# Optimization experiments

Measured on AMD Instinct MI355X. Metric: run time of the kernel, lower is better.

Reference implementation:

```python
import jax, jax.numpy as jnp
import numpy as np

NUM_HEADS = 16
DIM = 1024
HARMONICS = 32
B, L = 2, 2048


def holo_linear(x, basis, phase, amp):
    # x: [B,L,in]; basis: [H,in] (L2-normalized rows); phase/amp: [out,H]
    # Original builds complex(res,0) * amp*exp(i*phase) and takes real of sum
    # over harmonics -> sum_h res_h * amp[o,h]*cos(phase[o,h]).
    resonance = jnp.einsum('bli,hi->blh', x, basis)        # [B,L,H]
    w = amp * jnp.cos(phase)                               # [out,H]
    return jnp.einsum('blh,oh->blo', resonance, w)         # [B,L,out]


def setup_inputs() -> dict:
    key = jax.random.key(0)
    ks = jax.random.split(key, 13)
    two_pi = 2.0 * np.pi

    def make_proj(k0, k1):
        basis = jax.random.normal(k0, (HARMONICS, DIM), dtype=jnp.float32)
        basis = basis / jnp.linalg.norm(basis, axis=1, keepdims=True)
        phase = jax.random.normal(k1, (DIM, HARMONICS), dtype=jnp.float32) * two_pi
        amp = jnp.ones((DIM, HARMONICS), dtype=jnp.float32) / HARMONICS
        return basis, phase, amp

    x = jax.random.normal(ks[0], (B, L, DIM), dtype=jnp.float32)
    bq, pq, aq = make_proj(ks[1], ks[2])
    bk, pk, ak = make_proj(ks[3], ks[4])
    bv, pv, av = make_proj(ks[5], ks[6])
    bo, po, ao = make_proj(ks[7], ks[8])
    return {
        'x': x,
        'basis_q': bq, 'phase_q': pq, 'amp_q': aq,
        'basis_k': bk, 'phase_k': pk, 'amp_k': ak,
        'basis_v': bv, 'phase_v': pv, 'amp_v': av,
        'basis_o': bo, 'phase_o': po, 'amp_o': ao,
    }


def reference(x, basis_q, phase_q, amp_q, basis_k, phase_k, amp_k,
              basis_v, phase_v, amp_v, basis_o, phase_o, amp_o):
    Bsz, Ls, C = x.shape
    head_dim = C // NUM_HEADS
    scale = head_dim ** (-0.5)

    def split_heads(t):  # [B,L,C] -> [B,H,L,hd]
        return t.reshape(Bsz, Ls, NUM_HEADS, head_dim).transpose(0, 2, 1, 3)

    q = split_heads(holo_linear(x, basis_q, phase_q, amp_q))
    k = split_heads(holo_linear(x, basis_k, phase_k, amp_k))
    v = split_heads(holo_linear(x, basis_v, phase_v, amp_v))

    attn = jnp.einsum('bhqd,bhkd->bhqk', q, k) * scale      # [B,H,L,L]
    attn = jax.nn.softmax(attn, axis=-1)
    out = jnp.einsum('bhqk,bhkd->bhqd', attn, v)            # [B,H,L,hd]
    out = out.transpose(0, 2, 1, 3).reshape(Bsz, Ls, C)
    return holo_linear(out, basis_o, phase_o, amp_o)
```

## Files before the change

### kernel.cpp

```cpp
#include <hip/hip_runtime.h>
#include <hip/hip_bf16.h>
#include <cstdint>
#include <cstddef>

#define NH   16
#define HD   64
#define CD   1024
#define HARM 32
#define BSZ  2
#define LSEQ 2048
#define NROW (BSZ*LSEQ)

typedef __attribute__((ext_vector_type(8))) short short8;
typedef __attribute__((ext_vector_type(16))) float float16v;

__device__ inline ushort bf16u(float f) {
    __hip_bfloat16 h = __float2bfloat16(f);
    return *(ushort*)&h;
}
__device__ inline float ubf(ushort u) {
    return __uint_as_float((unsigned)u << 16);
}
__device__ inline unsigned pk2(float a, float b) {
    return (unsigned)bf16u(a) | ((unsigned)bf16u(b) << 16);
}
__device__ inline int crow(int r, int half) { return (r & 3) + 8 * (r >> 2) + 4 * half; }

union S8U { short8 v; uint2 u[2]; };

__device__ inline short8 pk_frag(const unsigned* pk, int cc) {
    S8U o;
    o.u[0] = make_uint2(pk[4 * cc + 0], pk[4 * cc + 1]);
    o.u[1] = make_uint2(pk[4 * cc + 2], pk[4 * cc + 3]);
    return o.v;
}

__global__ void prep_kern(const float* __restrict__ bq, const float* __restrict__ bk,
                          const float* __restrict__ bv, const float* __restrict__ bo,
                          const float* __restrict__ pq, const float* __restrict__ aq,
                          const float* __restrict__ pk, const float* __restrict__ ak,
                          const float* __restrict__ pv, const float* __restrict__ av,
                          const float* __restrict__ po, const float* __restrict__ ao,
                          ushort* __restrict__ bF, ushort* __restrict__ wqkvF,
                          ushort* __restrict__ wobF) {
    const float QSCALE = 0.125f * 1.44269504088896340736f;
    unsigned tid = blockIdx.x * 256 + threadIdx.x;
    if (tid < 16384) {
        unsigned l31 = tid & 31, h = (tid >> 5) & 1, kc = (tid >> 6) & 63, proj = tid >> 12;
        const float* bp = (proj == 0) ? bq : (proj == 1) ? bk : (proj == 2) ? bv : bo;
        const float* s = bp + (size_t)l31 * CD + kc * 16;
        unsigned o0 = (proj == 3) ? h * 4 : h * 8;
        unsigned o1 = o0 + ((proj == 3) ? 8 : 4);
        float4 f0 = *(const float4*)(s + o0), f1 = *(const float4*)(s + o1);
        S8U o;
        o.u[0] = make_uint2(pk2(f0.x, f0.y), pk2(f0.z, f0.w));
        o.u[1] = make_uint2(pk2(f1.x, f1.y), pk2(f1.z, f1.w));
        *(short8*)(bF + (size_t)tid * 8) = o.v;
        return;
    }
    if (tid < 28672) {
        unsigned i = tid - 16384;
        unsigned l31 = i & 31, h = (i >> 5) & 1, kc2 = (i >> 6) & 1;
        unsigned ntp = (i >> 7) & 31, proj = i >> 12;
        const float* ph = (proj == 0) ? pq : (proj == 1) ? pk : pv;
        const float* am = (proj == 0) ? aq : (proj == 1) ? ak : av;
        float sc = (proj == 0) ? QSCALE : 1.0f;
        size_t s = (size_t)(ntp * 32 + l31) * HARM + kc2 * 16 + h * 4;
        float4 p0 = *(const float4*)(ph + s), p1 = *(const float4*)(ph + s + 8);
        float4 a0 = *(const float4*)(am + s), a1 = *(const float4*)(am + s + 8);
        S8U o;
        o.u[0] = make_uint2(pk2(a0.x * cosf(p0.x) * sc, a0.y * cosf(p0.y) * sc),
                            pk2(a0.z * cosf(p0.z) * sc, a0.w * cosf(p0.w) * sc));
        o.u[1] = make_uint2(pk2(a1.x * cosf(p1.x) * sc, a1.y * cosf(p1.y) * sc),
                            pk2(a1.z * cosf(p1.z) * sc, a1.w * cosf(p1.w) * sc));
        *(short8*)(wqkvF + (size_t)i * 8) = o.v;
        return;
    }
    {
        unsigned i = tid - 28672;
        unsigned l31 = i & 31, h = (i >> 5) & 1, kc2 = (i >> 6) & 1, nt = i >> 7;
        size_t s = (size_t)(nt * 32 + l31) * HARM + kc2 * 16 + h * 4;
        float4 p0 = *(const float4*)(po + s), p1 = *(const float4*)(po + s + 8);
        float4 a0 = *(const float4*)(ao + s), a1 = *(const float4*)(ao + s + 8);
        S8U o;
        o.u[0] = make_uint2(pk2(a0.x * cosf(p0.x), a0.y * cosf(p0.y)),
                            pk2(a0.z * cosf(p0.z), a0.w * cosf(p0.w)));
        o.u[1] = make_uint2(pk2(a1.x * cosf(p1.x), a1.y * cosf(p1.y)),
                            pk2(a1.z * cosf(p1.z), a1.w * cosf(p1.w)));
        *(short8*)(wobF + (size_t)i * 8) = o.v;
    }
}

__global__ __launch_bounds__(256) void res_part_kern(const float* __restrict__ x,
                                                     const ushort* __restrict__ bF,
                                                     float* __restrict__ respart) {
    __shared__ ushort xs[32 * 256];
    __shared__ float red[4 * 16 * 64];
    const int t = threadIdx.x, wave = t >> 6, lane = t & 63;
    const int l31 = lane & 31, h = lane >> 5;
    const int kseg = blockIdx.x & 3, rg = blockIdx.x >> 2;
    const int n0 = rg * 32;

#pragma unroll
    for (int i = 0; i < 8; i++) {
        int idx = i * 256 + t, row = idx >> 6, c4 = idx & 63;
        float4 v = *(const float4*)(x + (size_t)(n0 + row) * CD + kseg * 256 + c4 * 4);
        int chunk = (c4 >> 1) ^ (row & 15), sub = c4 & 1;
        *(ushort4*)(&xs[row * 256 + chunk * 8 + sub * 4]) =
            make_ushort4(bf16u(v.x), bf16u(v.y), bf16u(v.z), bf16u(v.w));
    }
    __syncthreads();

    float16v resC[3] = {};
#pragma unroll
    for (int kci = 0; kci < 4; kci++) {
        int c = wave * 8 + kci * 2 + h;
        short8 bx = *(const short8*)(&xs[l31 * 256 + (c ^ (l31 & 15)) * 8]);
        int kcg = kseg * 16 + wave * 4 + kci;
#pragma unroll
        for (int p = 0; p < 3; p++) {
            short8 a = *(const short8*)(bF + ((size_t)((p * 64 + kcg) * 2 + h) * 32 + l31) * 8);
            resC[p] = __builtin_amdgcn_mfma_f32_32x32x16_bf16(a, bx, resC[p], 0, 0, 0);
        }
    }
    float* outb = respart + ((size_t)(kseg * 128 + rg) * 3) * 1024;
    for (int p = 0; p < 3; p++) {
        __syncthreads();
#pragma unroll
        for (int r = 0; r < 16; r++) red[wave * 1024 + r * 64 + lane] = resC[p][r];
        __syncthreads();
#pragma unroll
        for (int i = 0; i < 4; i++) {
            int e = i * 256 + t;
            outb[p * 1024 + e] = (red[e] + red[1024 + e]) + (red[2048 + e] + red[3072 + e]);
        }
    }
}

__global__ __launch_bounds__(256) void rp_kern(const float* __restrict__ respart,
                                               unsigned* __restrict__ rfbuf) {
    const int tid = blockIdx.x * 256 + threadIdx.x;
    const int rest = tid / 384, u = tid % 384;
    const int p = u >> 7, cc = (u >> 6) & 1, lane = u & 63;

    const float* base = respart + ((size_t)rest * 3 + p) * 1024 + cc * 512 + lane;
    unsigned w[4];
#pragma unroll
    for (int q = 0; q < 4; q++) {
        const float* pa = base + (2 * q) * 64;
        const float* pb = pa + 64;
        float a = (pa[0] + pa[393216]) + (pa[2 * 393216] + pa[3 * 393216]);
        float bv_ = (pb[0] + pb[393216]) + (pb[2 * 393216] + pb[3 * 393216]);
        w[q] = pk2(a, bv_);
    }
    *(uint4*)(rfbuf + (size_t)rest * 1536 + ((p * 2 + cc) * 64 + lane) * 4) =
        make_uint4(w[0], w[1], w[2], w[3]);
}

__global__ __launch_bounds__(256) void qkv_kern(const unsigned* __restrict__ rfbuf,
                                                const ushort* __restrict__ wqkvF,
                                                ushort* __restrict__ qtile,
                                                ushort* __restrict__ ktile,
                                                ushort* __restrict__ vtile) {
    const int t = threadIdx.x, wave = t >> 6, lane = t & 63;
    const int l31 = lane & 31, h = lane >> 5;
    const int ntg = blockIdx.x % 24, rest = blockIdx.x / 24;
    const int b = rest >> 6, l0q = rest & 63;
    const int nt = ntg * 4 + wave;
    const int proj = nt >> 5, ntp = nt & 31;
    const int head = ntp >> 1, sub = ntp & 1;
    const int kblk = l0q >> 1, mtk = l0q & 1;

    const unsigned* rb = rfbuf + (size_t)rest * 1536 + ((proj * 2) * 64 + lane) * 4;
    uint4 q0 = *(const uint4*)(rb);
    uint4 q1 = *(const uint4*)(rb + 256);
    S8U r0, r1;
    r0.u[0] = make_uint2(q0.x, q0.y); r0.u[1] = make_uint2(q0.z, q0.w);
    r1.u[0] = make_uint2(q1.x, q1.y); r1.u[1] = make_uint2(q1.z, q1.w);

    const ushort* wp = wqkvF + ((size_t)(proj * 32 + ntp) * 4) * 256;
    short8 wf0 = *(const short8*)(wp + (size_t)h * 256 + l31 * 8);
    short8 wf1 = *(const short8*)(wp + (size_t)(2 + h) * 256 + l31 * 8);
    float16v c = {};
    if (proj < 2) {
        c = __builtin_amdgcn_mfma_f32_32x32x16_bf16(wf0, r0.v, c, 0, 0, 0);
        c = __builtin_amdgcn_mfma_f32_32x32x16_bf16(wf1, r1.v, c, 0, 0, 0);
    } else {
        c = __builtin_amdgcn_mfma_f32_32x32x16_bf16(r0.v, wf0, c, 0, 0, 0);
        c = __builtin_amdgcn_mfma_f32_32x32x16_bf16(r1.v, wf1, c, 0, 0, 0);
    }
    unsigned pkc[8];
#pragma unroll
    for (int j = 0; j < 8; j++) pkc[j] = pk2(c[2 * j], c[2 * j + 1]);

    if (proj == 0) {
        ushort* base = qtile + (((size_t)(b * NH + head) * 64 + l0q)) * 2048;
#pragma unroll
        for (int cc = 0; cc < 2; cc++)
            *(short8*)(base + (sub * 2 + cc) * 512 + h * 256 + l31 * 8) =
                pk_frag(pkc, cc);
    } else if (proj == 1) {
        ushort* base = ktile + ((size_t)(b * NH + head) * 32 + kblk) * 4096 + mtk * 2048;
#pragma unroll
        for (int cc = 0; cc < 2; cc++)
            *(short8*)(base + (sub * 2 + cc) * 512 + h * 256 + l31 * 8) =
                pk_frag(pkc, cc);
    } else {
        ushort* base = vtile + ((size_t)(b * NH + head) * 32 + kblk) * 4096 + sub * 2048;
#pragma unroll
        for (int cc = 0; cc < 2; cc++)
            *(short8*)(base + (mtk * 2 + cc) * 512 + h * 256 + l31 * 8) =
                pk_frag(pkc, cc);
    }
}

__global__ __launch_bounds__(256, 2) void flash8(const ushort* __restrict__ qtile,
                                                 const ushort* __restrict__ ktile,
                                                 const ushort* __restrict__ vtile,
                                                 ushort* __restrict__ Opart,
                                                 float* __restrict__ lbuf) {
    __shared__ ushort kb[2][4096];
    __shared__ ushort vb[2][4096];
    const int t = threadIdx.x;
    const int wave = t >> 6, lane = t & 63;
    const int l31 = lane & 31, h = lane >> 5;
    const int d = blockIdx.x;
    const int logical = (d & 7) * 64 + (d >> 3);
    const int bh = logical >> 4;
    const int inner = logical & 15;
    const int ksp = inner >> 3;
    const int qtg = inner & 7;
    const int qt0 = qtg * 8 + wave * 2;
    const int fo = h * 256 + l31 * 8;
    const int so = t * 8;

    const ushort* qtb = qtile + ((size_t)bh * 64 + qt0) * 2048;
    short8 qfa[4], qfb[4];
#pragma unroll
    for (int kc = 0; kc < 4; kc++) {
        qfa[kc] = *(const short8*)(qtb + kc * 512 + fo);
        qfb[kc] = *(const short8*)(qtb + 2048 + kc * 512 + fo);
    }

    const ushort* ktb = ktile + (size_t)bh * 32 * 4096;
    const ushort* vtb = vtile + (size_t)bh * 32 * 4096;
    const int k0 = ksp * 16;

    {
        const ushort* ks = ktb + (size_t)k0 * 4096;
        const ushort* vs = vtb + (size_t)k0 * 4096;
        short8 a0 = *(const short8*)(ks + so);
        short8 a1 = *(const short8*)(ks + 2048 + so);
        short8 b0 = *(const short8*)(vs + so);
        short8 b1 = *(const short8*)(vs + 2048 + so);
        *(short8*)(kb[0] + so) = a0; *(short8*)(kb[0] + 2048 + so) = a1;
        *(short8*)(vb[0] + so) = b0; *(short8*)(vb[0] + 2048 + so) = b1;
    }
    __syncthreads();

    S8U ones;
    ones.u[0] = make_uint2(0x3F803F80u, 0x3F803F80u);
    ones.u[1] = make_uint2(0x3F803F80u, 0x3F803F80u);

    float16v O0a = {}, O1a = {}, Laa = {};
    float16v O0b = {}, O1b = {}, Lab = {};

#pragma unroll
    for (int it = 0; it < 16; it++) {
        const int cur = it & 1, nxt = cur ^ 1;

        short8 a0, a1, b0, b1;
        if (it < 15) {
            const ushort* ks = ktb + (size_t)(k0 + it + 1) * 4096;
            const ushort* vs = vtb + (size_t)(k0 + it + 1) * 4096;
            a0 = *(const short8*)(ks + so);
            a1 = *(const short8*)(ks + 2048 + so);
            b0 = *(const short8*)(vs + so);
            b1 = *(const short8*)(vs + 2048 + so);
        }

        short8 kf[2][4];
#pragma unroll
        for (int mt = 0; mt < 2; mt++)
#pragma unroll
            for (int kc = 0; kc < 4; kc++)
                kf[mt][kc] = *(const short8*)(kb[cur] + mt * 2048 + kc * 512 + fo);
        float16v s0a = {}, s1a = {}, s0b = {}, s1b = {};
#pragma unroll
        for (int kc = 0; kc < 4; kc++) {
            s0a = __builtin_amdgcn_mfma_f32_32x32x16_bf16(kf[0][kc], qfa[kc], s0a, 0, 0, 0);
            s1a = __builtin_amdgcn_mfma_f32_32x32x16_bf16(kf[1][kc], qfa[kc], s1a, 0, 0, 0);
            s0b = __builtin_amdgcn_mfma_f32_32x32x16_bf16(kf[0][kc], qfb[kc], s0b, 0, 0, 0);
            s1b = __builtin_amdgcn_mfma_f32_32x32x16_bf16(kf[1][kc], qfb[kc], s1b, 0, 0, 0);
        }
        short8 vf[2][4];
#pragma unroll
        for (int mt = 0; mt < 2; mt++)
#pragma unroll
            for (int kc = 0; kc < 4; kc++)
                vf[mt][kc] = *(const short8*)(vb[cur] + mt * 2048 + kc * 512 + fo);

        unsigned pk0a[8], pk1a[8], pk0b[8], pk1b[8];
#pragma unroll
        for (int j2 = 0; j2 < 8; j2++) {
            pk0a[j2] = pk2(__builtin_amdgcn_exp2f(s0a[2 * j2]),
                           __builtin_amdgcn_exp2f(s0a[2 * j2 + 1]));
            pk1a[j2] = pk2(__builtin_amdgcn_exp2f(s1a[2 * j2]),
                           __builtin_amdgcn_exp2f(s1a[2 * j2 + 1]));
            pk0b[j2] = pk2(__builtin_amdgcn_exp2f(s0b[2 * j2]),
                           __builtin_amdgcn_exp2f(s0b[2 * j2 + 1]));
            pk1b[j2] = pk2(__builtin_amdgcn_exp2f(s1b[2 * j2]),
                           __builtin_amdgcn_exp2f(s1b[2 * j2 + 1]));
        }
#pragma unroll
        for (int kc = 0; kc < 4; kc++) {
            const unsigned* pma = (kc < 2) ? pk0a : pk1a;
            const unsigned* pmb = (kc < 2) ? pk0b : pk1b;
            short8 bfa = pk_frag(pma, kc & 1);
            short8 bfb = pk_frag(pmb, kc & 1);
            Laa = __builtin_amdgcn_mfma_f32_32x32x16_bf16(ones.v, bfa, Laa, 0, 0, 0);
            O0a = __builtin_amdgcn_mfma_f32_32x32x16_bf16(vf[0][kc], bfa, O0a, 0, 0, 0);
            O1a = __builtin_amdgcn_mfma_f32_32x32x16_bf16(vf[1][kc], bfa, O1a, 0, 0, 0);
            Lab = __builtin_amdgcn_mfma_f32_32x32x16_bf16(ones.v, bfb, Lab, 0, 0, 0);
            O0b = __builtin_amdgcn_mfma_f32_32x32x16_bf16(vf[0][kc], bfb, O0b, 0, 0, 0);
            O1b = __builtin_amdgcn_mfma_f32_32x32x16_bf16(vf[1][kc], bfb, O1b, 0, 0, 0);
        }

        if (it < 15) {
            *(short8*)(kb[nxt] + so) = a0; *(short8*)(kb[nxt] + 2048 + so) = a1;
            *(short8*)(vb[nxt] + so) = b0; *(short8*)(vb[nxt] + 2048 + so) = b1;
        }
        __syncthreads();
    }

    if (h == 0) {
        lbuf[(size_t)ksp * 65536 + bh * 2048 + qt0 * 32 + l31] = Laa[0];
        lbuf[(size_t)ksp * 65536 + bh * 2048 + (qt0 + 1) * 32 + l31] = Lab[0];
    }
#pragma unroll
    for (int j = 0; j < 2; j++) {
        ushort* ob = Opart + (size_t)ksp * 4194304 + ((size_t)bh * 64 + qt0 + j) * 2048;
#pragma unroll
        for (int mt = 0; mt < 2; mt++) {
            float16v Ov = j ? (mt ? O1b : O0b) : (mt ? O1a : O0a);
            unsigned pkO[8];
#pragma unroll
            for (int j2 = 0; j2 < 8; j2++) pkO[j2] = pk2(Ov[2 * j2], Ov[2 * j2 + 1]);
#pragma unroll
            for (int cc = 0; cc < 2; cc++)
                *(short8*)(ob + ((mt * 2 + cc) * 2 + h) * 256 + l31 * 8) =
                    pk_frag(pkO, cc);
        }
    }
}

__global__ __launch_bounds__(256) void back1_kern(const ushort* __restrict__ Opart,
                                                  const float* __restrict__ lbuf,
                                                  const ushort* __restrict__ bF,
                                                  float* __restrict__ respart2) {
    __shared__ float red[4 * 16 * 64];
    const int t = threadIdx.x, wave = t >> 6, lane = t & 63;
    const int l31 = lane & 31, h = lane >> 5;
    const int hq = blockIdx.x & 3, rg = blockIdx.x >> 2;
    const int b = rg >> 6, qt = rg & 63;
    const int hd = hq * 4 + wave, bh = b * NH + hd;

    float lb = lbuf[(size_t)bh * 2048 + qt * 32 + l31] +
               lbuf[(size_t)65536 + (size_t)bh * 2048 + qt * 32 + l31];
    float invl = 1.0f / lb;
    const ushort* ob0 = Opart + ((size_t)bh * 64 + qt) * 2048;
    const ushort* ob1 = ob0 + 4194304;

    float16v c = {};
#pragma unroll
    for (int kc = 0; kc < 4; kc++) {
        short8 o0 = *(const short8*)(ob0 + (kc * 2 + h) * 256 + l31 * 8);
        short8 o1 = *(const short8*)(ob1 + (kc * 2 + h) * 256 + l31 * 8);
        float av[8];
#pragma unroll
        for (int e = 0; e < 8; e++)
            av[e] = (ubf((ushort)o0[e]) + ubf((ushort)o1[e])) * invl;
        S8U bn;
        bn.u[0] = make_uint2(pk2(av[0], av[1]), pk2(av[2], av[3]));
        bn.u[1] = make_uint2(pk2(av[4], av[5]), pk2(av[6], av[7]));
        int kcg = hd * 4 + kc;
        short8 a = *(const short8*)(bF + ((size_t)((3 * 64 + kcg) * 2 + h) * 32 + l31) * 8);
        c = __builtin_amdgcn_mfma_f32_32x32x16_bf16(a, bn.v, c, 0, 0, 0);
    }
#pragma unroll
    for (int r = 0; r < 16; r++) red[wave * 1024 + r * 64 + lane] = c[r];
    __syncthreads();
#pragma unroll
    for (int i = 0; i < 4; i++) {
        int e = i * 256 + t;
        respart2[((size_t)hq * 128 + rg) * 1024 + e] =
            (red[e] + red[1024 + e]) + (red[2048 + e] + red[3072 + e]);
    }
}

__global__ __launch_bounds__(256) void back2_kern(const float* __restrict__ respart2,
                                                  const ushort* __restrict__ wobF,
                                                  float* __restrict__ out) {
    const int t = threadIdx.x, wave = t >> 6, lane = t & 63;
    const int l31 = lane & 31, h = lane >> 5;
    const int ng = blockIdx.x & 7, rg = blockIdx.x >> 3;

    float cf[16];
#pragma unroll
    for (int r = 0; r < 16; r++) {
        const float* pp = respart2 + r * 64 + lane;
        cf[r] = (pp[(size_t)rg * 1024] + pp[(size_t)(128 + rg) * 1024]) +
                (pp[(size_t)(256 + rg) * 1024] + pp[(size_t)(384 + rg) * 1024]);
    }
    unsigned pkr[8];
#pragma unroll
    for (int j = 0; j < 8; j++) pkr[j] = pk2(cf[2 * j], cf[2 * j + 1]);
    short8 a0 = pk_frag(pkr, 0);
    short8 a1 = pk_frag(pkr, 1);

    int nt = ng * 4 + wave;
    const ushort* wp = wobF + (size_t)nt * 1024;
    short8 wf0 = *(const short8*)(wp + (size_t)h * 256 + l31 * 8);
    short8 wf1 = *(const short8*)(wp + (size_t)(2 + h) * 256 + l31 * 8);
    float16v co = {};
    co = __builtin_amdgcn_mfma_f32_32x32x16_bf16(a0, wf0, co, 0, 0, 0);
    co = __builtin_amdgcn_mfma_f32_32x32x16_bf16(a1, wf1, co, 0, 0, 0);
#pragma unroll
    for (int r = 0; r < 16; r++) {
        int row = rg * 32 + crow(r, h);
        out[(size_t)row * CD + nt * 32 + l31] = co[r];
    }
}

extern "C" void kernel_launch(void* const* d_in, const int* in_sizes, int n_in,
                              void* d_out, int out_size, void* d_ws, size_t ws_size,
                              hipStream_t stream) {
    const float* x  = (const float*)d_in[0];
    const float* bq = (const float*)d_in[1];
    const float* pq = (const float*)d_in[2];
    const float* aq = (const float*)d_in[3];
    const float* bk = (const float*)d_in[4];
    const float* pk = (const float*)d_in[5];
    const float* ak = (const float*)d_in[6];
    const float* bv = (const float*)d_in[7];
    const float* pv = (const float*)d_in[8];
    const float* av = (const float*)d_in[9];
    const float* bo = (const float*)d_in[10];
    const float* po = (const float*)d_in[11];
    const float* ao = (const float*)d_in[12];

    char* ws = (char*)d_ws;
    ushort* bF      = (ushort*)(ws + 0);
    ushort* wqkvF   = (ushort*)(ws + 262144);
    ushort* wobF    = (ushort*)(ws + 458752);
    ushort* qtile   = (ushort*)(ws + 524288);
    ushort* ktile   = (ushort*)(ws + 8912896);
    ushort* vtile   = (ushort*)(ws + 17301504);
    ushort* Opart   = (ushort*)(ws + 25690112);
    float*  lbuf    = (float*)(ws + 42467328);
    float*  respart = (float*)(ws + 42991616);
    float*  respart2= (float*)(ws + 524288);
    unsigned* rfbuf = (unsigned*)(ws + 25690112);

    prep_kern<<<128, 256, 0, stream>>>(bq, bk, bv, bo, pq, aq, pk, ak, pv, av,
                                       po, ao, bF, wqkvF, wobF);
    res_part_kern<<<512, 256, 0, stream>>>(x, bF, respart);
    rp_kern<<<192, 256, 0, stream>>>(respart, rfbuf);
    qkv_kern<<<3072, 256, 0, stream>>>(rfbuf, wqkvF, qtile, ktile, vtile);
    flash8<<<512, 256, 0, stream>>>(qtile, ktile, vtile, Opart, lbuf);
    back1_kern<<<512, 256, 0, stream>>>(Opart, lbuf, bF, respart2);
    back2_kern<<<1024, 256, 0, stream>>>(respart2, wobF, (float*)d_out);
}
```

Baseline: 151.6 us.

## Software-pipeline QK^T one tile ahead of exp and PV in attention loop

Restructures the attention inner loop so the S=K·Q MFMAs for tile it+1 are issued before the exp2/pack and P·V MFMAs of tile it, keeping K one stage further ahead in the LDS double buffer. The goal is to overlap transcendental/VALU softmax work with matrix-core work and hide the dependency between the score MFMAs and the exp. It costs two extra sets of score accumulators (more VGPRs), adds a prologue, and changes the buffer indexing, which risks register pressure or spills.

Result: slower. 325.1 us (+114.4%).

```diff
diff --git a/kernel.cpp b/kernel.cpp
--- a/kernel.cpp
+++ b/kernel.cpp
@@ -262,56 +262,89 @@
     ones.u[0] = make_uint2(0x3F803F80u, 0x3F803F80u);
     ones.u[1] = make_uint2(0x3F803F80u, 0x3F803F80u);
 
+    float16v sS[2][4];
+    {
+        short8 ka0, ka1;
+        {
+            const ushort* ks = ktb + (size_t)(k0 + 1) * 4096;
+            ka0 = *(const short8*)(ks + so);
+            ka1 = *(const short8*)(ks + 2048 + so);
+        }
+        short8 kf[2][4];
+#pragma unroll
+        for (int mt = 0; mt < 2; mt++)
+#pragma unroll
+            for (int kc = 0; kc < 4; kc++)
+                kf[mt][kc] = *(const short8*)(kb[0] + mt * 2048 + kc * 512 + fo);
+#pragma unroll
+        for (int j = 0; j < 4; j++) sS[0][j] = (float16v){};
+#pragma unroll
+        for (int kc = 0; kc < 4; kc++) {
+            sS[0][0] = __builtin_amdgcn_mfma_f32_32x32x16_bf16(kf[0][kc], qfa[kc], sS[0][0], 0, 0, 0);
+            sS[0][1] = __builtin_amdgcn_mfma_f32_32x32x16_bf16(kf[1][kc], qfa[kc], sS[0][1], 0, 0, 0);
+            sS[0][2] = __builtin_amdgcn_mfma_f32_32x32x16_bf16(kf[0][kc], qfb[kc], sS[0][2], 0, 0, 0);
+            sS[0][3] = __builtin_amdgcn_mfma_f32_32x32x16_bf16(kf[1][kc], qfb[kc], sS[0][3], 0, 0, 0);
+        }
+        *(short8*)(kb[1] + so) = ka0; *(short8*)(kb[1] + 2048 + so) = ka1;
+    }
+    __syncthreads();
+
     float16v O0a = {}, O1a = {}, Laa = {};
     float16v O0b = {}, O1b = {}, Lab = {};
 
 #pragma unroll
     for (int it = 0; it < 16; it++) {
-        const int cur = it & 1, nxt = cur ^ 1;
-
-        short8 a0, a1, b0, b1;
+        const int pc = it & 1, pn = pc ^ 1;
+
+        short8 ka0, ka1, va0, va1;
+        if (it < 14) {
+            const ushort* ks = ktb + (size_t)(k0 + it + 2) * 4096;
+            ka0 = *(const short8*)(ks + so);
+            ka1 = *(const short8*)(ks + 2048 + so);
+        }
         if (it < 15) {
-            const ushort* ks = ktb + (size_t)(k0 + it + 1) * 4096;
             const ushort* vs = vtb + (size_t)(k0 + it + 1) * 4096;
-            a0 = *(const short8*)(ks + so);
-            a1 = *(const short8*)(ks + 2048 + so);
-            b0 = *(const short8*)(vs + so);
-            b1 = *(const short8*)(vs + 2048 + so);
-        }
-
-        short8 kf[2][4];
+            va0 = *(const short8*)(vs + so);
+            va1 = *(const short8*)(vs + 2048 + so);
+        }
+
+        if (it < 15) {
+            short8 kf[2][4];
+#pragma unroll
+            for (int mt = 0; mt < 2; mt++)
+#pragma unroll
+                for (int kc = 0; kc < 4; kc++)
+                    kf[mt][kc] = *(const short8*)(kb[pn] + mt * 2048 + kc * 512 + fo);
+#pragma unroll
+            for (int j = 0; j < 4; j++) sS[pn][j] = (float16v){};
+#pragma unroll
+            for (int kc = 0; kc < 4; kc++) {
+                sS[pn][0] = __builtin_amdgcn_mfma_f32_32x32x16_bf16(kf[0][kc], qfa[kc], sS[pn][0], 0, 0, 0);
+                sS[pn][1] = __builtin_amdgcn_mfma_f32_32x32x16_bf16(kf[1][kc], qfa[kc], sS[pn][1], 0, 0, 0);
+                sS[pn][2] = __builtin_amdgcn_mfma_f32_32x32x16_bf16(kf[0][kc], qfb[kc], sS[pn][2], 0, 0, 0);
+                sS[pn][3] = __builtin_amdgcn_mfma_f32_32x32x16_bf16(kf[1][kc], qfb[kc], sS[pn][3], 0, 0, 0);
+            }
+        }
+
+        unsigned pk0a[8], pk1a[8], pk0b[8], pk1b[8];
+#pragma unroll
+        for (int j2 = 0; j2 < 8; j2++) {
+            pk0a[j2] = pk2(__builtin_amdgcn_exp2f(sS[pc][0][2 * j2]),
+                           __builtin_amdgcn_exp2f(sS[pc][0][2 * j2 + 1]));
+            pk1a[j2] = pk2(__builtin_amdgcn_exp2f(sS[pc][1][2 * j2]),
+                           __builtin_amdgcn_exp2f(sS[pc][1][2 * j2 + 1]));
+            pk0b[j2] = pk2(__builtin_amdgcn_exp2f(sS[pc][2][2 * j2]),
+                           __builtin_amdgcn_exp2f(sS[pc][2][2 * j2 + 1]));
+            pk1b[j2] = pk2(__builtin_amdgcn_exp2f(sS[pc][3][2 * j2]),
+                           __builtin_amdgcn_exp2f(sS[pc][3][2 * j2 + 1]));
+        }
+
+        short8 vf[2][4];
 #pragma unroll
         for (int mt = 0; mt < 2; mt++)
 #pragma unroll
             for (int kc = 0; kc < 4; kc++)
-                kf[mt][kc] = *(const short8*)(kb[cur] + mt * 2048 + kc * 512 + fo);
-        float16v s0a = {}, s1a = {}, s0b = {}, s1b = {};
-#pragma unroll
-        for (int kc = 0; kc < 4; kc++) {
-            s0a = __builtin_amdgcn_mfma_f32_32x32x16_bf16(kf[0][kc], qfa[kc], s0a, 0, 0, 0);
-            s1a = __builtin_amdgcn_mfma_f32_32x32x16_bf16(kf[1][kc], qfa[kc], s1a, 0, 0, 0);
-            s0b = __builtin_amdgcn_mfma_f32_32x32x16_bf16(kf[0][kc], qfb[kc], s0b, 0, 0, 0);
-            s1b = __builtin_amdgcn_mfma_f32_32x32x16_bf16(kf[1][kc], qfb[kc], s1b, 0, 0, 0);
-        }
-        short8 vf[2][4];
-#pragma unroll
-        for (int mt = 0; mt < 2; mt++)
-#pragma unroll
-            for (int kc = 0; kc < 4; kc++)
-                vf[mt][kc] = *(const short8*)(vb[cur] + mt * 2048 + kc * 512 + fo);
-
-        unsigned pk0a[8], pk1a[8], pk0b[8], pk1b[8];
-#pragma unroll
-        for (int j2 = 0; j2 < 8; j2++) {
-            pk0a[j2] = pk2(__builtin_amdgcn_exp2f(s0a[2 * j2]),
-                           __builtin_amdgcn_exp2f(s0a[2 * j2 + 1]));
-            pk1a[j2] = pk2(__builtin_amdgcn_exp2f(s1a[2 * j2]),
-                           __builtin_amdgcn_exp2f(s1a[2 * j2 + 1]));
-            pk0b[j2] = pk2(__builtin_amdgcn_exp2f(s0b[2 * j2]),
-                           __builtin_amdgcn_exp2f(s0b[2 * j2 + 1]));
-            pk1b[j2] = pk2(__builtin_amdgcn_exp2f(s1b[2 * j2]),
-                           __builtin_amdgcn_exp2f(s1b[2 * j2 + 1]));
-        }
+                vf[mt][kc] = *(const short8*)(vb[pc] + mt * 2048 + kc * 512 + fo);
 #pragma unroll
         for (int kc = 0; kc < 4; kc++) {
             const unsigned* pma = (kc < 2) ? pk0a : pk1a;
@@ -326,11 +359,13 @@
             O1b = __builtin_amdgcn_mfma_f32_32x32x16_bf16(vf[1][kc], bfb, O1b, 0, 0, 0);
         }
 
+        if (it < 14) {
+            *(short8*)(kb[pc] + so) = ka0; *(short8*)(kb[pc] + 2048 + so) = ka1;
+        }
         if (it < 15) {
-            *(short8*)(kb[nxt] + so) = a0; *(short8*)(kb[nxt] + 2048 + so) = a1;
-            *(short8*)(vb[nxt] + so) = b0; *(short8*)(vb[nxt] + 2048 + so) = b1;
-        }
-        __syncthreads();
+            *(short8*)(vb[pn] + so) = va0; *(short8*)(vb[pn] + 2048 + so) = va1;
+            __syncthreads();
+        }
     }
 
     if (h == 0) {
```

## Fuse resonance partial GEMM and split-K reduction into one kernel

Applied to the files above, without the earlier changes.

Merges the split-K resonance projection kernel and its separate reduction kernel into a single 512-thread kernel per 32-row group. Each block now covers the full 1024-wide K dimension across 8 waves and reduces the per-wave partial sums in shared memory before writing packed bf16 results. This removes one launch and the global round trip of the fp32 partial buffer. In exchange there are only 128 blocks instead of 512, which lowers parallelism across CUs, and the final reduction runs on just 128 threads.

After: 151.7 us. No clear change (+0.0%).

```diff
diff --git a/kernel.cpp b/kernel.cpp
--- a/kernel.cpp
+++ b/kernel.cpp
@@ -91,70 +91,66 @@
     }
 }
 
-__global__ __launch_bounds__(256) void res_part_kern(const float* __restrict__ x,
-                                                     const ushort* __restrict__ bF,
-                                                     float* __restrict__ respart) {
-    __shared__ ushort xs[32 * 256];
-    __shared__ float red[4 * 16 * 64];
+__global__ __launch_bounds__(512) void resrp_kern(const float* __restrict__ x,
+                                                  const ushort* __restrict__ bF,
+                                                  unsigned* __restrict__ rfbuf) {
+    __shared__ ushort xs[4][8192];
+    float* red = (float*)xs;
     const int t = threadIdx.x, wave = t >> 6, lane = t & 63;
     const int l31 = lane & 31, h = lane >> 5;
-    const int kseg = blockIdx.x & 3, rg = blockIdx.x >> 2;
-    const int n0 = rg * 32;
-
-#pragma unroll
-    for (int i = 0; i < 8; i++) {
-        int idx = i * 256 + t, row = idx >> 6, c4 = idx & 63;
+    const int rest = blockIdx.x;
+    const int n0 = rest * 32;
+
+#pragma unroll
+    for (int i = 0; i < 16; i++) {
+        int idx = i * 512 + t;
+        int row = idx >> 8, c4g = idx & 255;
+        int kseg = c4g >> 6, c4 = c4g & 63;
         float4 v = *(const float4*)(x + (size_t)(n0 + row) * CD + kseg * 256 + c4 * 4);
         int chunk = (c4 >> 1) ^ (row & 15), sub = c4 & 1;
-        *(ushort4*)(&xs[row * 256 + chunk * 8 + sub * 4]) =
+        *(ushort4*)(&xs[kseg][row * 256 + chunk * 8 + sub * 4]) =
             make_ushort4(bf16u(v.x), bf16u(v.y), bf16u(v.z), bf16u(v.w));
     }
     __syncthreads();
 
     float16v resC[3] = {};
 #pragma unroll
-    for (int kci = 0; kci < 4; kci++) {
-        int c = wave * 8 + kci * 2 + h;
-        short8 bx = *(const short8*)(&xs[l31 * 256 + (c ^ (l31 & 15)) * 8]);
-        int kcg = kseg * 16 + wave * 4 + kci;
+    for (int i = 0; i < 8; i++) {
+        int kcg = wave * 8 + i;
+        int kseg = kcg >> 4, m = kcg & 15;
+        int c = m * 2 + h;
+        short8 bx = *(const short8*)(&xs[kseg][l31 * 256 + ((c ^ (l31 & 15)) * 8)]);
 #pragma unroll
         for (int p = 0; p < 3; p++) {
             short8 a = *(const short8*)(bF + ((size_t)((p * 64 + kcg) * 2 + h) * 32 + l31) * 8);
             resC[p] = __builtin_amdgcn_mfma_f32_32x32x16_bf16(a, bx, resC[p], 0, 0, 0);
         }
     }
-    float* outb = respart + ((size_t)(kseg * 128 + rg) * 3) * 1024;
+
+    unsigned* ob = rfbuf + (size_t)rest * 1536;
     for (int p = 0; p < 3; p++) {
         __syncthreads();
 #pragma unroll
         for (int r = 0; r < 16; r++) red[wave * 1024 + r * 64 + lane] = resC[p][r];
         __syncthreads();
-#pragma unroll
-        for (int i = 0; i < 4; i++) {
-            int e = i * 256 + t;
-            outb[p * 1024 + e] = (red[e] + red[1024 + e]) + (red[2048 + e] + red[3072 + e]);
-        }
-    }
-}
-
-__global__ __launch_bounds__(256) void rp_kern(const float* __restrict__ respart,
-                                               unsigned* __restrict__ rfbuf) {
-    const int tid = blockIdx.x * 256 + threadIdx.x;
-    const int rest = tid / 384, u = tid % 384;
-    const int p = u >> 7, cc = (u >> 6) & 1, lane = u & 63;
-
-    const float* base = respart + ((size_t)rest * 3 + p) * 1024 + cc * 512 + lane;
-    unsigned w[4];
-#pragma unroll
-    for (int q = 0; q < 4; q++) {
-        const float* pa = base + (2 * q) * 64;
-        const float* pb = pa + 64;
-        float a = (pa[0] + pa[393216]) + (pa[2 * 393216] + pa[3 * 393216]);
-        float bv_ = (pb[0] + pb[393216]) + (pb[2 * 393216] + pb[3 * 393216]);
-        w[q] = pk2(a, bv_);
-    }
-    *(uint4*)(rfbuf + (size_t)rest * 1536 + ((p * 2 + cc) * 64 + lane) * 4) =
-        make_uint4(w[0], w[1], w[2], w[3]);
+        if (t < 128) {
+            int cc = t >> 6, ln = t & 63;
+            unsigned w[4];
+#pragma unroll
+            for (int q = 0; q < 4; q++) {
+                int j = cc * 4 + q;
+                float va = 0.0f, vb2 = 0.0f;
+#pragma unroll
+                for (int wv = 0; wv < 8; wv++) {
+                    va  += red[wv * 1024 + (2 * j) * 64 + ln];
+                    vb2 += red[wv * 1024 + (2 * j + 1) * 64 + ln];
+                }
+                w[q] = pk2(va, vb2);
+            }
+            *(uint4*)(ob + ((p * 2 + cc) * 64 + ln) * 4) =
+                make_uint4(w[0], w[1], w[2], w[3]);
+        }
+    }
 }
 
 __global__ __launch_bounds__(256) void qkv_kern(const unsigned* __restrict__ rfbuf,
@@ -458,14 +454,12 @@
     ushort* vtile   = (ushort*)(ws + 17301504);
     ushort* Opart   = (ushort*)(ws + 25690112);
     float*  lbuf    = (float*)(ws + 42467328);
-    float*  respart = (float*)(ws + 42991616);
     float*  respart2= (float*)(ws + 524288);
     unsigned* rfbuf = (unsigned*)(ws + 25690112);
 
     prep_kern<<<128, 256, 0, stream>>>(bq, bk, bv, bo, pq, aq, pk, ak, pv, av,
                                        po, ao, bF, wqkvF, wobF);
-    res_part_kern<<<512, 256, 0, stream>>>(x, bF, respart);
-    rp_kern<<<192, 256, 0, stream>>>(respart, rfbuf);
+    resrp_kern<<<128, 512, 0, stream>>>(x, bF, rfbuf);
     qkv_kern<<<3072, 256, 0, stream>>>(rfbuf, wqkvF, qtile, ktile, vtile);
     flash8<<<512, 256, 0, stream>>>(qtile, ktile, vtile, Opart, lbuf);
     back1_kern<<<512, 256, 0, stream>>>(Opart, lbuf, bF, respart2);
```
